# Kernel optimization log

Hardware: AMD Instinct MI355X
Metric: run time of the kernel (lower is better)

## Reference

```python
import jax, jax.numpy as jnp
import numpy as np

N_PE = 100000   # num 'pe' nodes
N_R = 100000    # num 'router' nodes
E = 600000      # edges per relation
D_IN = 64       # input feature dim per node type
H = 128         # hidden_channels
G = 64          # graphs in batch


def setup_inputs() -> dict:
    key = jax.random.key(0)
    ks = jax.random.split(key, 20)
    inp = {}
    inp["x_pe"] = jax.random.normal(ks[0], (N_PE, D_IN), jnp.float32)
    inp["x_r"] = jax.random.normal(ks[1], (N_R, D_IN), jnp.float32)
    # edge_index per relation: row0 = src node ids, row1 = dst node ids
    inp["ei_per"] = jax.random.randint(ks[2], (2, E), 0, N_PE, jnp.int32)   # pe -> router
    inp["ei_rpe"] = jax.random.randint(ks[3], (2, E), 0, N_R, jnp.int32)    # router -> pe
    inp["ei_rr"] = jax.random.randint(ks[4], (2, E), 0, N_R, jnp.int32)     # router -> router
    inp["batch_pe"] = jnp.sort(jax.random.randint(ks[5], (N_PE,), 0, G, jnp.int32))
    inp["batch_r"] = jnp.sort(jax.random.randint(ks[6], (N_R,), 0, G, jnp.int32))
    # GraphConv params, relation axis ordered [pe->router, router->pe, router->router]
    s1 = 1.0 / np.sqrt(D_IN)
    s2 = 1.0 / np.sqrt(H)
    inp["Wrel1"] = jax.random.normal(ks[7], (3, D_IN, H), jnp.float32) * s1
    inp["brel1"] = jnp.zeros((3, H), jnp.float32)
    inp["Wroot1"] = jax.random.normal(ks[8], (3, D_IN, H), jnp.float32) * s1
    inp["Wrel23"] = jax.random.normal(ks[9], (2, 3, H, H), jnp.float32) * s2
    inp["brel23"] = jnp.zeros((2, 3, H), jnp.float32)
    inp["Wroot23"] = jax.random.normal(ks[10], (2, 3, H, H), jnp.float32) * s2
    # per-node-type MLP heads, type axis ordered [pe, router]
    inp["mlp_W1"] = jax.random.normal(ks[11], (2, H, 5), jnp.float32) * s2
    inp["mlp_b1"] = jnp.zeros((2, 5), jnp.float32)
    inp["mlp_W2"] = jax.random.normal(ks[12], (2, 5, 1), jnp.float32) * (1.0 / np.sqrt(5.0))
    inp["mlp_b2"] = jnp.zeros((2, 1), jnp.float32)
    inp["out_W"] = jax.random.normal(ks[13], (2, 1), jnp.float32) * (1.0 / np.sqrt(2.0))
    inp["out_b"] = jnp.zeros((1,), jnp.float32)
    return inp


def _hetero_graphconv(x_pe, x_r, ei_per, ei_rpe, ei_rr, Wrel, brel, Wroot):
    # GraphConv: lin_rel(scatter_add(x_src)) + lin_root(x_dst); to_hetero sums per dst type.
    agg_r_from_pe = jax.ops.segment_sum(x_pe[ei_per[0]], ei_per[1], num_segments=N_R)
    agg_pe_from_r = jax.ops.segment_sum(x_r[ei_rpe[0]], ei_rpe[1], num_segments=N_PE)
    agg_r_from_r = jax.ops.segment_sum(x_r[ei_rr[0]], ei_rr[1], num_segments=N_R)
    o_pe = agg_pe_from_r @ Wrel[1] + brel[1] + x_pe @ Wroot[1]
    o_r = (agg_r_from_pe @ Wrel[0] + brel[0] + x_r @ Wroot[0]) \
        + (agg_r_from_r @ Wrel[2] + brel[2] + x_r @ Wroot[2])
    return o_pe, o_r


def reference(x_pe, x_r, ei_per, ei_rpe, ei_rr, batch_pe, batch_r,
              Wrel1, brel1, Wroot1, Wrel23, brel23, Wroot23,
              mlp_W1, mlp_b1, mlp_W2, mlp_b2, out_W, out_b):
    h_pe, h_r = _hetero_graphconv(x_pe, x_r, ei_per, ei_rpe, ei_rr, Wrel1, brel1, Wroot1)
    h_pe, h_r = jax.nn.relu(h_pe), jax.nn.relu(h_r)
    h_pe, h_r = _hetero_graphconv(h_pe, h_r, ei_per, ei_rpe, ei_rr, Wrel23[0], brel23[0], Wroot23[0])
    h_pe, h_r = jax.nn.relu(h_pe), jax.nn.relu(h_r)
    h_pe, h_r = _hetero_graphconv(h_pe, h_r, ei_per, ei_rpe, ei_rr, Wrel23[1], brel23[1], Wroot23[1])
    gm_pe = jax.ops.segment_max(h_pe, batch_pe, num_segments=G)  # [G, H]
    gm_r = jax.ops.segment_max(h_r, batch_r, num_segments=G)
    def mlp(x, W1, b1, W2, b2):
        return jax.nn.relu(x @ W1 + b1) @ W2 + b2
    o_pe = mlp(gm_pe, mlp_W1[0], mlp_b1[0], mlp_W2[0], mlp_b2[0])  # [G, 1]
    o_r = mlp(gm_r, mlp_W1[1], mlp_b1[1], mlp_W2[1], mlp_b2[1])
    cat = jnp.concatenate([o_pe, o_r], axis=1)  # [G, 2]
    return cat @ out_W + out_b  # [G, 1]
```

## Files before the change

kernel.cpp:

```cpp
#include <hip/hip_runtime.h>
#include <cstddef>
#include <cstdint>

#define DIN 64
#define HID 128
#define NBKMAX 256
#define EPB 2048

typedef _Float16 half4v __attribute__((ext_vector_type(4)));
typedef _Float16 half8v __attribute__((ext_vector_type(8)));
typedef float f32x16 __attribute__((ext_vector_type(16)));

__device__ __forceinline__ unsigned encf(float f) {
    unsigned b = __float_as_uint(f);
    return (b & 0x80000000u) ? ~b : (b | 0x80000000u);
}
__device__ __forceinline__ float decf(unsigned u) {
    unsigned b = (u & 0x80000000u) ? (u & 0x7FFFFFFFu) : ~u;
    return __uint_as_float(b);
}

__global__ void conv_x2_k(const float* s0, _Float16* d0, int n40,
                          const float* s1, _Float16* d1, int n41) {
    int r = blockIdx.y;
    const float* s = r == 0 ? s0 : s1;
    _Float16* d = r == 0 ? d0 : d1;
    int n4 = r == 0 ? n40 : n41;
    int i = blockIdx.x * 256 + threadIdx.x;
    if (i >= n4) return;
    float4 v = *reinterpret_cast<const float4*>(&s[i * 4]);
    half4v h;
    h.x = (_Float16)v.x; h.y = (_Float16)v.y; h.z = (_Float16)v.z; h.w = (_Float16)v.w;
    *reinterpret_cast<half4v*>(&d[i * 4]) = h;
}

struct CW { const float* src; const float* src2; _Float16* dst; int K; int total; };
__global__ void conv_w8_k(CW c0, CW c1, CW c2, CW c3, CW c4, CW c5, CW c6, CW c7) {
    CW J;
    switch (blockIdx.y) {
        case 0: J = c0; break; case 1: J = c1; break; case 2: J = c2; break;
        case 3: J = c3; break; case 4: J = c4; break; case 5: J = c5; break;
        case 6: J = c6; break; default: J = c7; break;
    }
    int i = blockIdx.x * 256 + threadIdx.x;
    if (i >= J.total) return;
    int m = i / (J.K * HID);
    int rem = i % (J.K * HID);
    int k = rem / HID;
    int col = rem % HID;
    float v = J.src[i];
    if (J.src2) v += J.src2[i];
    J.dst[(size_t)m * HID * J.K + (size_t)col * J.K + k] = (_Float16)v;
}

__global__ __launch_bounds__(256) void bhist_k(const int* e0, const int* e1, const int* e2, int E,
                                               int* c0, int* c1, int* c2) {
    int r = blockIdx.y;
    const int* ei = r == 0 ? e0 : (r == 1 ? e1 : e2);
    int* cnt = r == 0 ? c0 : (r == 1 ? c1 : c2);
    __shared__ int sc[NBKMAX];
    int t = threadIdx.x;
    sc[t] = 0;
    __syncthreads();
    int base = blockIdx.x * EPB;
    int n = min(EPB, E - base);
    for (int i = t; i < n; i += 256)
        atomicAdd(&sc[(unsigned)ei[E + base + i] >> 9], 1);
    __syncthreads();
    if (sc[t]) atomicAdd(&cnt[t], sc[t]);
}

__global__ __launch_bounds__(256) void bscan_k(int* c0, int* bb0, int* cu0, int* rp0, int n0,
                                               int* c1, int* bb1, int* cu1, int* rp1, int n1,
                                               int* c2, int* bb2, int* cu2, int* rp2, int n2,
                                               int E) {
    __shared__ int sh[256];
    int t = threadIdx.x;
    for (int r = 0; r < 3; ++r) {
        int* cnt = r == 0 ? c0 : (r == 1 ? c1 : c2);
        int* bb  = r == 0 ? bb0 : (r == 1 ? bb1 : bb2);
        int* cu  = r == 0 ? cu0 : (r == 1 ? cu1 : cu2);
        int* rp  = r == 0 ? rp0 : (r == 1 ? rp1 : rp2);
        int N    = r == 0 ? n0 : (r == 1 ? n1 : n2);
        int v = cnt[t];
        sh[t] = v;
        __syncthreads();
        for (int off = 1; off < 256; off <<= 1) {
            int val = (t >= off) ? sh[t - off] : 0;
            __syncthreads();
            sh[t] += val;
            __syncthreads();
        }
        int ex = sh[t] - v;
        bb[t] = ex;
        cu[t] = ex;
        if (t == 255) bb[256] = sh[255];
        if (t == 0) rp[N] = E;
        __syncthreads();
    }
}

__global__ __launch_bounds__(256) void bin_k(const int* e0, const int* e1, const int* e2, int E,
                                             int* cu0, int* cu1, int* cu2,
                                             unsigned* t0, unsigned* t1, unsigned* t2) {
    int r = blockIdx.y;
    const int* ei = r == 0 ? e0 : (r == 1 ? e1 : e2);
    int* gcur = r == 0 ? cu0 : (r == 1 ? cu1 : cu2);
    unsigned* temp = r == 0 ? t0 : (r == 1 ? t1 : t2);
    __shared__ unsigned pk[EPB];
    __shared__ unsigned short bkb[EPB];
    __shared__ int cnt[NBKMAX];
    __shared__ int scn[NBKMAX];
    __shared__ int rb[NBKMAX];
    int t = threadIdx.x;
    int base = blockIdx.x * EPB;
    int n = min(EPB, E - base);
    cnt[t] = 0;
    __syncthreads();
    for (int i = t; i < n; i += 256)
        atomicAdd(&cnt[(unsigned)ei[E + base + i] >> 9], 1);
    __syncthreads();
    {
        int v = cnt[t];
        scn[t] = v;
        __syncthreads();
        for (int off = 1; off < 256; off <<= 1) {
            int val = (t >= off) ? scn[t - off] : 0;
            __syncthreads();
            scn[t] += val;
            __syncthreads();
        }
        int ex = scn[t] - v;
        __syncthreads();
        scn[t] = ex;
    }
    {
        int c = cnt[t];
        rb[t] = c ? atomicAdd(&gcur[t], c) : 0;
        cnt[t] = 0;
    }
    __syncthreads();
    for (int i = t; i < n; i += 256) {
        int s = ei[base + i];
        int d = ei[E + base + i];
        int b = (unsigned)d >> 9;
        int slot = scn[b] + atomicAdd(&cnt[b], 1);
        pk[slot] = ((unsigned)s << 9) | (unsigned)(d & 511);
        bkb[slot] = (unsigned short)b;
    }
    __syncthreads();
    for (int i = t; i < n; i += 256) {
        int b = bkb[i];
        temp[rb[b] + (i - scn[b])] = pk[i];
    }
}

__global__ __launch_bounds__(256) void bcsr_k(const unsigned* t0, const unsigned* t1, const unsigned* t2,
                                              const int* bb0, const int* bb1, const int* bb2,
                                              int* rp0, int* rp1, int* rp2,
                                              int* a0, int* a1, int* a2,
                                              int n0, int n1, int n2) {
    int r = blockIdx.y;
    const unsigned* temp = r == 0 ? t0 : (r == 1 ? t1 : t2);
    const int* bb = r == 0 ? bb0 : (r == 1 ? bb1 : bb2);
    int* rp = r == 0 ? rp0 : (r == 1 ? rp1 : rp2);
    int* adj = r == 0 ? a0 : (r == 1 ? a1 : a2);
    int N = r == 0 ? n0 : (r == 1 ? n1 : n2);
    int b = blockIdx.x;
    int lo = bb[b], hi = bb[b + 1];
    __shared__ int cnt[512];
    __shared__ int sh[256];
    int t = threadIdx.x;
    cnt[t] = 0; cnt[t + 256] = 0;
    __syncthreads();
    for (int i = lo + t; i < hi; i += 256)
        atomicAdd(&cnt[temp[i] & 511], 1);
    __syncthreads();
    int c0 = cnt[2 * t], c1 = cnt[2 * t + 1];
    sh[t] = c0 + c1;
    __syncthreads();
    for (int off = 1; off < 256; off <<= 1) {
        int v = (t >= off) ? sh[t - off] : 0;
        __syncthreads();
        sh[t] += v;
        __syncthreads();
    }
    int pairExcl = sh[t] - (c0 + c1);
    __syncthreads();
    int e0x = lo + pairExcl;
    int e1x = e0x + c0;
    cnt[2 * t] = e0x;
    cnt[2 * t + 1] = e1x;
    int nodeBase = b * 512;
    if (nodeBase + 2 * t < N) rp[nodeBase + 2 * t] = e0x;
    if (nodeBase + 2 * t + 1 < N) rp[nodeBase + 2 * t + 1] = e1x;
    __syncthreads();
    for (int i = lo + t; i < hi; i += 256) {
        unsigned p = temp[i];
        int pos = atomicAdd(&cnt[p & 511], 1);
        adj[pos] = p >> 9;
    }
}

struct AJob { const _Float16* X; const int* rp; const int* adj; _Float16* AGG; int N; int gb; };
template <int D>
__global__ __launch_bounds__(256) void gather3_k(AJob a0, AJob a1, AJob a2) {
    int b = blockIdx.x;
    AJob J;
    if (b < a0.gb) { J = a0; }
    else if (b < a0.gb + a1.gb) { J = a1; b -= a0.gb; }
    else { J = a2; b -= a0.gb + a1.gb; }
    constexpr int TPN = D / 8;
    constexpr int NPB = 256 / TPN;
    int node = b * NPB + threadIdx.x / TPN;
    int glane = threadIdx.x % TPN;
    if (node >= J.N) return;
    int a = J.rp[node], e1 = J.rp[node + 1];
    float acc[8] = {0.f, 0.f, 0.f, 0.f, 0.f, 0.f, 0.f, 0.f};
    for (int base = a; base < e1; base += TPN) {
        int idx = base + glane;
        int myAdj = (idx < e1) ? J.adj[idx] : 0;
        int cnt = min(TPN, e1 - base);
        int j = 0;
        for (; j + 4 <= cnt; j += 4) {
            int s0 = __shfl(myAdj, j, TPN);
            int s1 = __shfl(myAdj, j + 1, TPN);
            int s2 = __shfl(myAdj, j + 2, TPN);
            int s3 = __shfl(myAdj, j + 3, TPN);
            half8v v0 = *reinterpret_cast<const half8v*>(&J.X[(size_t)s0 * D + glane * 8]);
            half8v v1 = *reinterpret_cast<const half8v*>(&J.X[(size_t)s1 * D + glane * 8]);
            half8v v2 = *reinterpret_cast<const half8v*>(&J.X[(size_t)s2 * D + glane * 8]);
            half8v v3 = *reinterpret_cast<const half8v*>(&J.X[(size_t)s3 * D + glane * 8]);
#pragma unroll
            for (int i = 0; i < 8; ++i)
                acc[i] += (float)v0[i] + (float)v1[i] + (float)v2[i] + (float)v3[i];
        }
        for (; j < cnt; ++j) {
            int s0 = __shfl(myAdj, j, TPN);
            half8v v0 = *reinterpret_cast<const half8v*>(&J.X[(size_t)s0 * D + glane * 8]);
#pragma unroll
            for (int i = 0; i < 8; ++i) acc[i] += (float)v0[i];
        }
    }
    half8v o;
#pragma unroll
    for (int i = 0; i < 8; ++i) o[i] = (_Float16)acc[i];
    *reinterpret_cast<half8v*>(&J.AGG[(size_t)node * D + glane * 8]) = o;
}

struct GJob {
    const _Float16* A0; const _Float16* A1; const _Float16* A2;
    const _Float16* W0; const _Float16* W1; const _Float16* W2;
    const float* b0; const float* b1;
    _Float16* O;
    int N; int total; int gb;
};

template <bool RELU>
__global__ __launch_bounds__(256) void gemm2_k(GJob j0, GJob j1, int K, int lg) {
    const bool second = ((int)blockIdx.x >= j0.gb);
    const GJob J = second ? j1 : j0;
    const int bx = blockIdx.x - (second ? j0.gb : 0);
    __shared__ _Float16 Alds[128 * 64];
    __shared__ _Float16 Wlds[128 * 64];
    const int tid = threadIdx.x;
    const int lane = tid & 63;
    const int w = tid >> 6;
    const int wr = w & 1, wc = w >> 1;
    const int rowBase = bx * 128;

    f32x16 acc[2][2];
#pragma unroll
    for (int r = 0; r < 2; ++r)
#pragma unroll
        for (int c = 0; c < 2; ++c)
#pragma unroll
            for (int q = 0; q < 16; ++q) acc[r][c][q] = 0.0f;

    const _Float16* Ap[3] = {J.A0, J.A1, J.A2};

    const int row = tid & 127;
    const int kh = (tid >> 7) * 32;
    const int gr = rowBase + row;
    const bool rowOK = (gr < J.N);
    int offS[4];
#pragma unroll
    for (int j = 0; j < 4; ++j) {
        int t = (kh >> 4) + (j >> 1);
        int k8 = j & 1;
        offS[j] = (((row >> 5) * 4 + t) * 64 + (row & 31) + 32 * k8) * 8;
    }

    const int total = J.total;
    const int cmask = (1 << lg) - 1;

    auto ldA = [&](int c, half8v h[4]) {
        int s = c >> lg;
        int k0 = (c & cmask) * 64;
        half8v z = {};
        h[0] = z; h[1] = z; h[2] = z; h[3] = z;
        if (rowOK) {
            const _Float16* p = Ap[s] + (size_t)gr * K + k0 + kh;
#pragma unroll
            for (int j = 0; j < 4; ++j) h[j] = *reinterpret_cast<const half8v*>(p + j * 8);
        }
    };
    auto ldW = [&](int c, half8v h[4]) {
        int s = c >> lg;
        int k0 = (c & cmask) * 64;
        const _Float16* __restrict__ Wt = (s == 0) ? J.W0 : (s == 1 ? J.W1 : J.W2);
        const _Float16* p = Wt + (size_t)row * K + k0 + kh;
#pragma unroll
        for (int j = 0; j < 4; ++j) h[j] = *reinterpret_cast<const half8v*>(p + j * 8);
    };

    half8v ra[4], rw[4];
    ldA(0, ra); ldW(0, rw);
#pragma unroll
    for (int j = 0; j < 4; ++j) {
        *reinterpret_cast<half8v*>(&Alds[offS[j]]) = ra[j];
        *reinterpret_cast<half8v*>(&Wlds[offS[j]]) = rw[j];
    }
    __syncthreads();

    for (int c = 0; c < total; ++c) {
        const bool more = (c + 1 < total);
        if (more) { ldA(c + 1, ra); ldW(c + 1, rw); }
#pragma unroll
        for (int t = 0; t < 4; ++t) {
            half8v av[2], wv[2];
#pragma unroll
            for (int r = 0; r < 2; ++r)
                av[r] = *reinterpret_cast<const half8v*>(&Alds[(((wr * 2 + r) * 4 + t) * 64 + lane) * 8]);
#pragma unroll
            for (int cc = 0; cc < 2; ++cc)
                wv[cc] = *reinterpret_cast<const half8v*>(&Wlds[(((wc * 2 + cc) * 4 + t) * 64 + lane) * 8]);
#pragma unroll
            for (int r = 0; r < 2; ++r)
#pragma unroll
                for (int cc = 0; cc < 2; ++cc)
                    acc[r][cc] = __builtin_amdgcn_mfma_f32_32x32x16_f16(wv[cc], av[r], acc[r][cc], 0, 0, 0);
        }
        __syncthreads();
        if (more) {
#pragma unroll
            for (int j = 0; j < 4; ++j) {
                *reinterpret_cast<half8v*>(&Alds[offS[j]]) = ra[j];
                *reinterpret_cast<half8v*>(&Wlds[offS[j]]) = rw[j];
            }
            __syncthreads();
        }
    }

    const int half_ = lane >> 5;
#pragma unroll
    for (int r = 0; r < 2; ++r) {
        int node = rowBase + (wr * 2 + r) * 32 + (lane & 31);
        bool ok = (node < J.N);
        _Float16* orow = J.O + (size_t)node * HID;
#pragma unroll
        for (int cc = 0; cc < 2; ++cc) {
            int fbase = wc * 64 + cc * 32;
#pragma unroll
            for (int g = 0; g < 4; ++g) {
                int fmine = fbase + g * 8 + 4 * half_;
                float4 bv = *reinterpret_cast<const float4*>(&J.b0[fmine]);
                if (J.b1) {
                    float4 b2v = *reinterpret_cast<const float4*>(&J.b1[fmine]);
                    bv.x += b2v.x; bv.y += b2v.y; bv.z += b2v.z; bv.w += b2v.w;
                }
                union { half4v h; int i[2]; } m, p;
#pragma unroll
                for (int i = 0; i < 4; ++i) {
                    float v = acc[r][cc][g * 4 + i] + ((const float*)&bv)[i];
                    if (RELU) v = fmaxf(v, 0.f);
                    m.h[i] = (_Float16)v;
                }
                p.i[0] = __shfl_xor(m.i[0], 32);
                p.i[1] = __shfl_xor(m.i[1], 32);
                half4v lo = half_ ? p.h : m.h;
                half4v hi = half_ ? m.h : p.h;
                half8v outv;
#pragma unroll
                for (int i = 0; i < 4; ++i) { outv[i] = lo[i]; outv[4 + i] = hi[i]; }
                if (ok && ((g & 1) == half_))
                    *reinterpret_cast<half8v*>(&orow[fbase + g * 8]) = outv;
            }
        }
    }
}

__global__ void seg_bounds2_k(const int* b0, int n0, int* s0,
                              const int* b1, int n1, int* s1, int G) {
    int r = blockIdx.x;
    const int* batch = r == 0 ? b0 : b1;
    int n = r == 0 ? n0 : n1;
    int* starts = r == 0 ? s0 : s1;
    int g = threadIdx.x;
    if (g > G) return;
    int lo = 0, hi = n;
    while (lo < hi) {
        int mid = (lo + hi) >> 1;
        if (batch[mid] < g) lo = mid + 1; else hi = mid;
    }
    starts[g] = lo;
}

__global__ __launch_bounds__(128) void seg_max2_k(const _Float16* H0, const int* st0, unsigned* g0,
                                                  const _Float16* H1, const int* st1, unsigned* g1) {
    int z = blockIdx.z;
    const _Float16* Hf = z == 0 ? H0 : H1;
    const int* starts = z == 0 ? st0 : st1;
    unsigned* gmU = z == 0 ? g0 : g1;
    int g = blockIdx.x;
    int sub = blockIdx.y;
    int SUB = gridDim.y;
    int f = threadIdx.x;
    int s0 = starts[g], s1 = starts[g + 1];
    int len = s1 - s0;
    if (len <= 0) return;
    int chunk = (len + SUB - 1) / SUB;
    int a = s0 + sub * chunk;
    int b = min(a + chunk, s1);
    if (a >= b) return;
    float m = -__builtin_huge_valf();
    for (int n = a; n < b; ++n) m = fmaxf(m, (float)Hf[(size_t)n * HID + f]);
    atomicMax(&gmU[g * HID + f], encf(m));
}

__global__ void head_k(const unsigned* __restrict__ gmU_pe, const unsigned* __restrict__ gmU_r,
                       const float* __restrict__ W1, const float* __restrict__ b1,
                       const float* __restrict__ W2, const float* __restrict__ b2,
                       const float* __restrict__ oW, const float* __restrict__ ob,
                       float* __restrict__ out, int G) {
    int g = threadIdx.x;
    if (g >= G) return;
    float vals[2];
#pragma unroll
    for (int t = 0; t < 2; ++t) {
        const unsigned* gm = t ? gmU_r : gmU_pe;
        float z[5];
#pragma unroll
        for (int j = 0; j < 5; ++j) z[j] = b1[t * 5 + j];
        for (int f = 0; f < HID; ++f) {
            float x = decf(gm[g * HID + f]);
#pragma unroll
            for (int j = 0; j < 5; ++j) z[j] = fmaf(x, W1[t * HID * 5 + f * 5 + j], z[j]);
        }
        float o = b2[t];
#pragma unroll
        for (int j = 0; j < 5; ++j) o = fmaf(fmaxf(z[j], 0.f), W2[t * 5 + j], o);
        vals[t] = o;
    }
    out[g] = vals[0] * oW[0] + vals[1] * oW[1] + ob[0];
}

extern "C" void kernel_launch(void* const* d_in, const int* in_sizes, int n_in,
                              void* d_out, int out_size, void* d_ws, size_t ws_size,
                              hipStream_t stream) {
    const float* x_pe    = (const float*)d_in[0];
    const float* x_r     = (const float*)d_in[1];
    const int* ei_per    = (const int*)d_in[2];
    const int* ei_rpe    = (const int*)d_in[3];
    const int* ei_rr     = (const int*)d_in[4];
    const int* batch_pe  = (const int*)d_in[5];
    const int* batch_r   = (const int*)d_in[6];
    const float* Wrel1   = (const float*)d_in[7];
    const float* brel1   = (const float*)d_in[8];
    const float* Wroot1  = (const float*)d_in[9];
    const float* Wrel23  = (const float*)d_in[10];
    const float* brel23  = (const float*)d_in[11];
    const float* Wroot23 = (const float*)d_in[12];
    const float* mlp_W1  = (const float*)d_in[13];
    const float* mlp_b1  = (const float*)d_in[14];
    const float* mlp_W2  = (const float*)d_in[15];
    const float* mlp_b2  = (const float*)d_in[16];
    const float* out_W   = (const float*)d_in[17];
    const float* out_b   = (const float*)d_in[18];
    float* out = (float*)d_out;

    const int N_PE = in_sizes[0] / DIN;
    const int N_R  = in_sizes[1] / DIN;
    const int E    = in_sizes[2] / 2;
    const int G    = out_size;
    const int NMAX = (N_PE > N_R) ? N_PE : N_R;
    const size_t SZM = (size_t)NMAX * HID;

    _Float16* H1 = (_Float16*)d_ws;
    _Float16* H2 = H1 + SZM;
    _Float16* H3 = H2 + SZM;
    _Float16* H4 = H3 + SZM;
    _Float16* H5 = H4 + SZM;
    _Float16* xh_pe = H5 + SZM;
    _Float16* xh_r  = xh_pe + (size_t)N_PE * DIN;
    _Float16* wt_rel1    = xh_r + (size_t)N_R * DIN;
    _Float16* wt_root1pe = wt_rel1 + 3 * DIN * HID;
    _Float16* wt_wsum1   = wt_root1pe + DIN * HID;
    _Float16* wt_rel23   = wt_wsum1 + DIN * HID;
    _Float16* wt_root_l2 = wt_rel23 + 6 * HID * HID;
    _Float16* wt_root_l3 = wt_root_l2 + HID * HID;
    _Float16* wt_wsum2   = wt_root_l3 + HID * HID;
    _Float16* wt_wsum3   = wt_wsum2 + HID * HID;
    unsigned* gmU_pe = (unsigned*)(wt_wsum3 + HID * HID);
    unsigned* gmU_r  = gmU_pe + G * HID;
    int* starts_pe = (int*)(gmU_r + G * HID);
    int* starts_r  = starts_pe + (G + 1);
    int* bktCnt = starts_r + (G + 1);
    int* bb     = bktCnt + 3 * NBKMAX;
    int* gcur   = bb + 3 * (NBKMAX + 1);
    int* csr    = gcur + 3 * NBKMAX;
    const size_t relstride = (size_t)(NMAX + 1) + 2 * (size_t)E + 16;

    int* rp[3]; int* adjp[3]; unsigned* tmp[3];
    const int Nds[3] = {N_R, N_PE, N_R};
    for (int r = 0; r < 3; ++r) {
        int* rowptr = csr + (size_t)r * relstride;
        rp[r] = rowptr;
        adjp[r] = rowptr + (Nds[r] + 1);
        tmp[r] = (unsigned*)(adjp[r] + E);
    }

    const int gpe = (N_PE + 127) / 128, grr = (N_R + 127) / 128;

    {
        int n40 = N_PE * DIN / 4, n41 = N_R * DIN / 4;
        int nmax = n40 > n41 ? n40 : n41;
        dim3 g((nmax + 255) / 256, 2);
        conv_x2_k<<<g, 256, 0, stream>>>(x_pe, xh_pe, n40, x_r, xh_r, n41);
    }
    {
        CW c0{Wrel1, nullptr, wt_rel1, DIN, 3 * DIN * HID};
        CW c1{Wroot1 + 1 * DIN * HID, nullptr, wt_root1pe, DIN, DIN * HID};
        CW c2{Wroot1, Wroot1 + 2 * DIN * HID, wt_wsum1, DIN, DIN * HID};
        CW c3{Wrel23, nullptr, wt_rel23, HID, 6 * HID * HID};
        CW c4{Wroot23 + 1 * HID * HID, nullptr, wt_root_l2, HID, HID * HID};
        CW c5{Wroot23 + 4 * HID * HID, nullptr, wt_root_l3, HID, HID * HID};
        CW c6{Wroot23, Wroot23 + 2 * HID * HID, wt_wsum2, HID, HID * HID};
        CW c7{Wroot23 + 3 * HID * HID, Wroot23 + 5 * HID * HID, wt_wsum3, HID, HID * HID};
        dim3 g((6 * HID * HID + 255) / 256, 8);
        conv_w8_k<<<g, 256, 0, stream>>>(c0, c1, c2, c3, c4, c5, c6, c7);
    }
    {
        hipMemsetAsync(bktCnt, 0, 3 * NBKMAX * sizeof(int), stream);
        int eb = (E + EPB - 1) / EPB;
        dim3 gh(eb, 3);
        bhist_k<<<gh, 256, 0, stream>>>(ei_per, ei_rpe, ei_rr, E,
                                        bktCnt, bktCnt + NBKMAX, bktCnt + 2 * NBKMAX);
        bscan_k<<<1, 256, 0, stream>>>(
            bktCnt, bb, gcur, rp[0], Nds[0],
            bktCnt + NBKMAX, bb + (NBKMAX + 1), gcur + NBKMAX, rp[1], Nds[1],
            bktCnt + 2 * NBKMAX, bb + 2 * (NBKMAX + 1), gcur + 2 * NBKMAX, rp[2], Nds[2], E);
        bin_k<<<gh, 256, 0, stream>>>(ei_per, ei_rpe, ei_rr, E,
                                      gcur, gcur + NBKMAX, gcur + 2 * NBKMAX,
                                      tmp[0], tmp[1], tmp[2]);
        dim3 gc(NBKMAX, 3);
        bcsr_k<<<gc, 256, 0, stream>>>(tmp[0], tmp[1], tmp[2],
                                       bb, bb + (NBKMAX + 1), bb + 2 * (NBKMAX + 1),
                                       rp[0], rp[1], rp[2],
                                       adjp[0], adjp[1], adjp[2],
                                       Nds[0], Nds[1], Nds[2]);
    }

    {
        AJob a0{xh_r, rp[1], adjp[1], H1, N_PE, (N_PE + 31) / 32};
        AJob a1{xh_pe, rp[0], adjp[0], H2, N_R, (N_R + 31) / 32};
        AJob a2{xh_r, rp[2], adjp[2], H3, N_R, (N_R + 31) / 32};
        gather3_k<DIN><<<a0.gb + a1.gb + a2.gb, 256, 0, stream>>>(a0, a1, a2);
        GJob jp{H1, xh_pe, nullptr,
                wt_rel1 + 1 * DIN * HID, wt_root1pe, nullptr,
                brel1 + HID, nullptr, H4, N_PE, 2, gpe};
        GJob jr{H2, H3, xh_r,
                wt_rel1, wt_rel1 + 2 * DIN * HID, wt_wsum1,
                brel1, brel1 + 2 * HID, H5, N_R, 3, grr};
        gemm2_k<true><<<gpe + grr, 256, 0, stream>>>(jp, jr, DIN, 0);
    }
    {
        AJob a0{H5, rp[1], adjp[1], H1, N_PE, (N_PE + 15) / 16};
        AJob a1{H4, rp[0], adjp[0], H2, N_R, (N_R + 15) / 16};
        AJob a2{H5, rp[2], adjp[2], H3, N_R, (N_R + 15) / 16};
        gather3_k<HID><<<a0.gb + a1.gb + a2.gb, 256, 0, stream>>>(a0, a1, a2);
        GJob jp{H1, H4, nullptr,
                wt_rel23 + 1 * HID * HID, wt_root_l2, nullptr,
                brel23 + HID, nullptr, H1, N_PE, 2 * 2, gpe};
        GJob jr{H2, H3, H5,
                wt_rel23, wt_rel23 + 2 * HID * HID, wt_wsum2,
                brel23, brel23 + 2 * HID, H2, N_R, 3 * 2, grr};
        gemm2_k<true><<<gpe + grr, 256, 0, stream>>>(jp, jr, HID, 1);
    }
    {
        AJob a0{H2, rp[1], adjp[1], H3, N_PE, (N_PE + 15) / 16};
        AJob a1{H1, rp[0], adjp[0], H4, N_R, (N_R + 15) / 16};
        AJob a2{H2, rp[2], adjp[2], H5, N_R, (N_R + 15) / 16};
        gather3_k<HID><<<a0.gb + a1.gb + a2.gb, 256, 0, stream>>>(a0, a1, a2);
        GJob jp{H3, H1, nullptr,
                wt_rel23 + 4 * HID * HID, wt_root_l3, nullptr,
                brel23 + 4 * HID, nullptr, H3, N_PE, 2 * 2, gpe};
        GJob jr{H4, H5, H2,
                wt_rel23 + 3 * HID * HID, wt_rel23 + 5 * HID * HID, wt_wsum3,
                brel23 + 3 * HID, brel23 + 5 * HID, H4, N_R, 3 * 2, grr};
        gemm2_k<false><<<gpe + grr, 256, 0, stream>>>(jp, jr, HID, 1);
    }

    seg_bounds2_k<<<2, 128, 0, stream>>>(batch_pe, N_PE, starts_pe, batch_r, N_R, starts_r, G);
    hipMemsetAsync(gmU_pe, 0, 2 * (size_t)G * HID * sizeof(unsigned), stream);
    dim3 gs(G, 16, 2);
    seg_max2_k<<<gs, 128, 0, stream>>>(H3, starts_pe, gmU_pe, H4, starts_r, gmU_r);
    head_k<<<1, 64, 0, stream>>>(gmU_pe, gmU_r, mlp_W1, mlp_b1, mlp_W2, mlp_b2, out_W, out_b, out, G);
}
```

Baseline: 619.0 us.

## Fuse prep kernels and split GEMM tile across eight waves

Merges weight conversion, edge bucket histogram and segment-bounds search into a single prep kernel. Two memsets become one by moving the bucket counters next to the max buffers. The GEMM goes from 256 to 512 threads per 128x128 tile, so each wave owns a 64x32 sub-tile with two accumulators instead of four, which cuts register pressure and adds waves to hide latency. The cost is less reuse of each LDS fragment per wave and more barrier participants, with the same LDS footprint per block.

```diff
diff --git a/kernel.cpp b/kernel.cpp
--- a/kernel.cpp
+++ b/kernel.cpp
@@ -35,39 +35,59 @@
 }
 
 struct CW { const float* src; const float* src2; _Float16* dst; int K; int total; };
-__global__ void conv_w8_k(CW c0, CW c1, CW c2, CW c3, CW c4, CW c5, CW c6, CW c7) {
-    CW J;
-    switch (blockIdx.y) {
-        case 0: J = c0; break; case 1: J = c1; break; case 2: J = c2; break;
-        case 3: J = c3; break; case 4: J = c4; break; case 5: J = c5; break;
-        case 6: J = c6; break; default: J = c7; break;
-    }
-    int i = blockIdx.x * 256 + threadIdx.x;
-    if (i >= J.total) return;
-    int m = i / (J.K * HID);
-    int rem = i % (J.K * HID);
-    int k = rem / HID;
-    int col = rem % HID;
-    float v = J.src[i];
-    if (J.src2) v += J.src2[i];
-    J.dst[(size_t)m * HID * J.K + (size_t)col * J.K + k] = (_Float16)v;
-}
-
-__global__ __launch_bounds__(256) void bhist_k(const int* e0, const int* e1, const int* e2, int E,
-                                               int* c0, int* c1, int* c2) {
-    int r = blockIdx.y;
-    const int* ei = r == 0 ? e0 : (r == 1 ? e1 : e2);
-    int* cnt = r == 0 ? c0 : (r == 1 ? c1 : c2);
-    __shared__ int sc[NBKMAX];
-    int t = threadIdx.x;
-    sc[t] = 0;
-    __syncthreads();
-    int base = blockIdx.x * EPB;
-    int n = min(EPB, E - base);
-    for (int i = t; i < n; i += 256)
-        atomicAdd(&sc[(unsigned)ei[E + base + i] >> 9], 1);
-    __syncthreads();
-    if (sc[t]) atomicAdd(&cnt[t], sc[t]);
+__global__ __launch_bounds__(256) void prep_k(
+    CW c0, CW c1, CW c2, CW c3, CW c4, CW c5, CW c6, CW c7,
+    const int* e0, const int* e1, const int* e2, int E,
+    int* hc0, int* hc1, int* hc2,
+    const int* bpe, int npe, int* spe,
+    const int* brr, int nrr, int* srr, int G) {
+    int y = blockIdx.y;
+    if (y < 8) {
+        CW J;
+        switch (y) {
+            case 0: J = c0; break; case 1: J = c1; break; case 2: J = c2; break;
+            case 3: J = c3; break; case 4: J = c4; break; case 5: J = c5; break;
+            case 6: J = c6; break; default: J = c7; break;
+        }
+        int i = blockIdx.x * 256 + threadIdx.x;
+        if (i >= J.total) return;
+        int m = i / (J.K * HID);
+        int rem = i % (J.K * HID);
+        int k = rem / HID;
+        int col = rem % HID;
+        float v = J.src[i];
+        if (J.src2) v += J.src2[i];
+        J.dst[(size_t)m * HID * J.K + (size_t)col * J.K + k] = (_Float16)v;
+    } else if (y < 11) {
+        int r = y - 8;
+        const int* ei = r == 0 ? e0 : (r == 1 ? e1 : e2);
+        int* cnt = r == 0 ? hc0 : (r == 1 ? hc1 : hc2);
+        __shared__ int sc[NBKMAX];
+        int t = threadIdx.x;
+        sc[t] = 0;
+        __syncthreads();
+        int base = blockIdx.x * EPB;
+        if (base >= E) return;
+        int n = min(EPB, E - base);
+        for (int i = t; i < n; i += 256)
+            atomicAdd(&sc[(unsigned)ei[E + base + i] >> 9], 1);
+        __syncthreads();
+        if (sc[t]) atomicAdd(&cnt[t], sc[t]);
+    } else {
+        int r = blockIdx.x;
+        if (r >= 2) return;
+        const int* batch = r == 0 ? bpe : brr;
+        int n = r == 0 ? npe : nrr;
+        int* starts = r == 0 ? spe : srr;
+        int g = threadIdx.x;
+        if (g > G) return;
+        int lo = 0, hi = n;
+        while (lo < hi) {
+            int mid = (lo + hi) >> 1;
+            if (batch[mid] < g) lo = mid + 1; else hi = mid;
+        }
+        starts[g] = lo;
+    }
 }
 
 __global__ __launch_bounds__(256) void bscan_k(int* c0, int* bb0, int* cu0, int* rp0, int n0,
@@ -257,7 +277,7 @@
 };
 
 template <bool RELU>
-__global__ __launch_bounds__(256) void gemm2_k(GJob j0, GJob j1, int K, int lg) {
+__global__ __launch_bounds__(512) void gemm2_k(GJob j0, GJob j1, int K, int lg) {
     const bool second = ((int)blockIdx.x >= j0.gb);
     const GJob J = second ? j1 : j0;
     const int bx = blockIdx.x - (second ? j0.gb : 0);
@@ -266,58 +286,54 @@
     const int tid = threadIdx.x;
     const int lane = tid & 63;
     const int w = tid >> 6;
-    const int wr = w & 1, wc = w >> 1;
+    const int wr = w & 1;
+    const int wc = w >> 1;
     const int rowBase = bx * 128;
 
-    f32x16 acc[2][2];
+    f32x16 acc[2];
 #pragma unroll
     for (int r = 0; r < 2; ++r)
 #pragma unroll
-        for (int c = 0; c < 2; ++c)
-#pragma unroll
-            for (int q = 0; q < 16; ++q) acc[r][c][q] = 0.0f;
+        for (int q = 0; q < 16; ++q) acc[r][q] = 0.0f;
 
     const _Float16* Ap[3] = {J.A0, J.A1, J.A2};
 
     const int row = tid & 127;
-    const int kh = (tid >> 7) * 32;
+    const int kq = (tid >> 7) * 16;
     const int gr = rowBase + row;
     const bool rowOK = (gr < J.N);
-    int offS[4];
-#pragma unroll
-    for (int j = 0; j < 4; ++j) {
-        int t = (kh >> 4) + (j >> 1);
-        int k8 = j & 1;
-        offS[j] = (((row >> 5) * 4 + t) * 64 + (row & 31) + 32 * k8) * 8;
-    }
+    int offS[2];
+#pragma unroll
+    for (int j = 0; j < 2; ++j)
+        offS[j] = (((row >> 5) * 4 + (kq >> 4)) * 64 + (row & 31) + 32 * j) * 8;
 
     const int total = J.total;
     const int cmask = (1 << lg) - 1;
 
-    auto ldA = [&](int c, half8v h[4]) {
+    auto ldA = [&](int c, half8v h[2]) {
         int s = c >> lg;
         int k0 = (c & cmask) * 64;
         half8v z = {};
-        h[0] = z; h[1] = z; h[2] = z; h[3] = z;
+        h[0] = z; h[1] = z;
         if (rowOK) {
-            const _Float16* p = Ap[s] + (size_t)gr * K + k0 + kh;
-#pragma unroll
-            for (int j = 0; j < 4; ++j) h[j] = *reinterpret_cast<const half8v*>(p + j * 8);
+            const _Float16* p = Ap[s] + (size_t)gr * K + k0 + kq;
+            h[0] = *reinterpret_cast<const half8v*>(p);
+            h[1] = *reinterpret_cast<const half8v*>(p + 8);
         }
     };
-    auto ldW = [&](int c, half8v h[4]) {
+    auto ldW = [&](int c, half8v h[2]) {
         int s = c >> lg;
         int k0 = (c & cmask) * 64;
         const _Float16* __restrict__ Wt = (s == 0) ? J.W0 : (s == 1 ? J.W1 : J.W2);
-        const _Float16* p = Wt + (size_t)row * K + k0 + kh;
-#pragma unroll
-        for (int j = 0; j < 4; ++j) h[j] = *reinterpret_cast<const half8v*>(p + j * 8);
+        const _Float16* p = Wt + (size_t)row * K + k0 + kq;
+        h[0] = *reinterpret_cast<const half8v*>(p);
+        h[1] = *reinterpret_cast<const half8v*>(p + 8);
     };
 
-    half8v ra[4], rw[4];
+    half8v ra[2], rw[2];
     ldA(0, ra); ldW(0, rw);
 #pragma unroll
-    for (int j = 0; j < 4; ++j) {
+    for (int j = 0; j < 2; ++j) {
         *reinterpret_cast<half8v*>(&Alds[offS[j]]) = ra[j];
         *reinterpret_cast<half8v*>(&Wlds[offS[j]]) = rw[j];
     }
@@ -328,23 +344,18 @@
         if (more) { ldA(c + 1, ra); ldW(c + 1, rw); }
 #pragma unroll
         for (int t = 0; t < 4; ++t) {
-            half8v av[2], wv[2];
-#pragma unroll
-            for (int r = 0; r < 2; ++r)
-                av[r] = *reinterpret_cast<const half8v*>(&Alds[(((wr * 2 + r) * 4 + t) * 64 + lane) * 8]);
-#pragma unroll
-            for (int cc = 0; cc < 2; ++cc)
-                wv[cc] = *reinterpret_cast<const half8v*>(&Wlds[(((wc * 2 + cc) * 4 + t) * 64 + lane) * 8]);
-#pragma unroll
-            for (int r = 0; r < 2; ++r)
-#pragma unroll
-                for (int cc = 0; cc < 2; ++cc)
-                    acc[r][cc] = __builtin_amdgcn_mfma_f32_32x32x16_f16(wv[cc], av[r], acc[r][cc], 0, 0, 0);
+            half8v wv = *reinterpret_cast<const half8v*>(&Wlds[((wc * 4 + t) * 64 + lane) * 8]);
+#pragma unroll
+            for (int r = 0; r < 2; ++r) {
+                half8v av = *reinterpret_cast<const half8v*>(
+                    &Alds[(((wr * 2 + r) * 4 + t) * 64 + lane) * 8]);
+                acc[r] = __builtin_amdgcn_mfma_f32_32x32x16_f16(wv, av, acc[r], 0, 0, 0);
+            }
         }
         __syncthreads();
         if (more) {
 #pragma unroll
-            for (int j = 0; j < 4; ++j) {
+            for (int j = 0; j < 2; ++j) {
                 *reinterpret_cast<half8v*>(&Alds[offS[j]]) = ra[j];
                 *reinterpret_cast<half8v*>(&Wlds[offS[j]]) = rw[j];
             }
@@ -353,57 +364,38 @@
     }
 
     const int half_ = lane >> 5;
+    const int fbase = wc * 32;
 #pragma unroll
     for (int r = 0; r < 2; ++r) {
         int node = rowBase + (wr * 2 + r) * 32 + (lane & 31);
         bool ok = (node < J.N);
         _Float16* orow = J.O + (size_t)node * HID;
 #pragma unroll
-        for (int cc = 0; cc < 2; ++cc) {
-            int fbase = wc * 64 + cc * 32;
-#pragma unroll
-            for (int g = 0; g < 4; ++g) {
-                int fmine = fbase + g * 8 + 4 * half_;
-                float4 bv = *reinterpret_cast<const float4*>(&J.b0[fmine]);
-                if (J.b1) {
-                    float4 b2v = *reinterpret_cast<const float4*>(&J.b1[fmine]);
-                    bv.x += b2v.x; bv.y += b2v.y; bv.z += b2v.z; bv.w += b2v.w;
-                }
-                union { half4v h; int i[2]; } m, p;
-#pragma unroll
-                for (int i = 0; i < 4; ++i) {
-                    float v = acc[r][cc][g * 4 + i] + ((const float*)&bv)[i];
-                    if (RELU) v = fmaxf(v, 0.f);
-                    m.h[i] = (_Float16)v;
-                }
-                p.i[0] = __shfl_xor(m.i[0], 32);
-                p.i[1] = __shfl_xor(m.i[1], 32);
-                half4v lo = half_ ? p.h : m.h;
-                half4v hi = half_ ? m.h : p.h;
-                half8v outv;
-#pragma unroll
-                for (int i = 0; i < 4; ++i) { outv[i] = lo[i]; outv[4 + i] = hi[i]; }
-                if (ok && ((g & 1) == half_))
-                    *reinterpret_cast<half8v*>(&orow[fbase + g * 8]) = outv;
+        for (int g = 0; g < 4; ++g) {
+            int fmine = fbase + g * 8 + 4 * half_;
+            float4 bv = *reinterpret_cast<const float4*>(&J.b0[fmine]);
+            if (J.b1) {
+                float4 b2v = *reinterpret_cast<const float4*>(&J.b1[fmine]);
+                bv.x += b2v.x; bv.y += b2v.y; bv.z += b2v.z; bv.w += b2v.w;
             }
-        }
-    }
-}
-
-__global__ void seg_bounds2_k(const int* b0, int n0, int* s0,
-                              const int* b1, int n1, int* s1, int G) {
-    int r = blockIdx.x;
-    const int* batch = r == 0 ? b0 : b1;
-    int n = r == 0 ? n0 : n1;
-    int* starts = r == 0 ? s0 : s1;
-    int g = threadIdx.x;
-    if (g > G) return;
-    int lo = 0, hi = n;
-    while (lo < hi) {
-        int mid = (lo + hi) >> 1;
-        if (batch[mid] < g) lo = mid + 1; else hi = mid;
-    }
-    starts[g] = lo;
+            union { half4v h; int i[2]; } m, p;
+#pragma unroll
+            for (int i = 0; i < 4; ++i) {
+                float v = acc[r][g * 4 + i] + ((const float*)&bv)[i];
+                if (RELU) v = fmaxf(v, 0.f);
+                m.h[i] = (_Float16)v;
+            }
+            p.i[0] = __shfl_xor(m.i[0], 32);
+            p.i[1] = __shfl_xor(m.i[1], 32);
+            half4v lo = half_ ? p.h : m.h;
+            half4v hi = half_ ? m.h : p.h;
+            half8v outv;
+#pragma unroll
+            for (int i = 0; i < 4; ++i) { outv[i] = lo[i]; outv[4 + i] = hi[i]; }
+            if (ok && ((g & 1) == half_))
+                *reinterpret_cast<half8v*>(&orow[fbase + g * 8]) = outv;
+        }
+    }
 }
 
 __global__ __launch_bounds__(128) void seg_max2_k(const _Float16* H0, const int* st0, unsigned* g0,
@@ -503,10 +495,10 @@
     _Float16* wt_wsum3   = wt_wsum2 + HID * HID;
     unsigned* gmU_pe = (unsigned*)(wt_wsum3 + HID * HID);
     unsigned* gmU_r  = gmU_pe + G * HID;
-    int* starts_pe = (int*)(gmU_r + G * HID);
+    int* bktCnt = (int*)(gmU_r + G * HID);
+    int* starts_pe = bktCnt + 3 * NBKMAX;
     int* starts_r  = starts_pe + (G + 1);
-    int* bktCnt = starts_r + (G + 1);
-    int* bb     = bktCnt + 3 * NBKMAX;
+    int* bb     = starts_r + (G + 1);
     int* gcur   = bb + 3 * (NBKMAX + 1);
     int* csr    = gcur + 3 * NBKMAX;
     const size_t relstride = (size_t)(NMAX + 1) + 2 * (size_t)E + 16;
@@ -521,7 +513,9 @@
     }
 
     const int gpe = (N_PE + 127) / 128, grr = (N_R + 127) / 128;
-
+    const int eb = (E + EPB - 1) / EPB;
+
+    hipMemsetAsync(gmU_pe, 0, (2 * (size_t)G * HID + 3 * NBKMAX) * sizeof(int), stream);
     {
         int n40 = N_PE * DIN / 4, n41 = N_R * DIN / 4;
         int nmax = n40 > n41 ? n40 : n41;
@@ -537,19 +531,21 @@
         CW c5{Wroot23 + 4 * HID * HID, nullptr, wt_root_l3, HID, HID * HID};
         CW c6{Wroot23, Wroot23 + 2 * HID * HID, wt_wsum2, HID, HID * HID};
         CW c7{Wroot23 + 3 * HID * HID, Wroot23 + 5 * HID * HID, wt_wsum3, HID, HID * HID};
-        dim3 g((6 * HID * HID + 255) / 256, 8);
-        conv_w8_k<<<g, 256, 0, stream>>>(c0, c1, c2, c3, c4, c5, c6, c7);
-    }
-    {
-        hipMemsetAsync(bktCnt, 0, 3 * NBKMAX * sizeof(int), stream);
-        int eb = (E + EPB - 1) / EPB;
-        dim3 gh(eb, 3);
-        bhist_k<<<gh, 256, 0, stream>>>(ei_per, ei_rpe, ei_rr, E,
-                                        bktCnt, bktCnt + NBKMAX, bktCnt + 2 * NBKMAX);
+        int gx = (6 * HID * HID + 255) / 256;
+        if (eb > gx) gx = eb;
+        dim3 g(gx, 12);
+        prep_k<<<g, 256, 0, stream>>>(c0, c1, c2, c3, c4, c5, c6, c7,
+                                      ei_per, ei_rpe, ei_rr, E,
+                                      bktCnt, bktCnt + NBKMAX, bktCnt + 2 * NBKMAX,
+                                      batch_pe, N_PE, starts_pe,
+                                      batch_r, N_R, starts_r, G);
+    }
+    {
         bscan_k<<<1, 256, 0, stream>>>(
             bktCnt, bb, gcur, rp[0], Nds[0],
             bktCnt + NBKMAX, bb + (NBKMAX + 1), gcur + NBKMAX, rp[1], Nds[1],
             bktCnt + 2 * NBKMAX, bb + 2 * (NBKMAX + 1), gcur + 2 * NBKMAX, rp[2], Nds[2], E);
+        dim3 gh(eb, 3);
         bin_k<<<gh, 256, 0, stream>>>(ei_per, ei_rpe, ei_rr, E,
                                       gcur, gcur + NBKMAX, gcur + 2 * NBKMAX,
                                       tmp[0], tmp[1], tmp[2]);
@@ -572,7 +568,7 @@
         GJob jr{H2, H3, xh_r,
                 wt_rel1, wt_rel1 + 2 * DIN * HID, wt_wsum1,
                 brel1, brel1 + 2 * HID, H5, N_R, 3, grr};
-        gemm2_k<true><<<gpe + grr, 256, 0, stream>>>(jp, jr, DIN, 0);
+        gemm2_k<true><<<gpe + grr, 512, 0, stream>>>(jp, jr, DIN, 0);
     }
     {
         AJob a0{H5, rp[1], adjp[1], H1, N_PE, (N_PE + 15) / 16};
@@ -585,7 +581,7 @@
         GJob jr{H2, H3, H5,
                 wt_rel23, wt_rel23 + 2 * HID * HID, wt_wsum2,
                 brel23, brel23 + 2 * HID, H2, N_R, 3 * 2, grr};
-        gemm2_k<true><<<gpe + grr, 256, 0, stream>>>(jp, jr, HID, 1);
+        gemm2_k<true><<<gpe + grr, 512, 0, stream>>>(jp, jr, HID, 1);
     }
     {
         AJob a0{H2, rp[1], adjp[1], H3, N_PE, (N_PE + 15) / 16};
@@ -598,11 +594,9 @@
         GJob jr{H4, H5, H2,
                 wt_rel23 + 3 * HID * HID, wt_rel23 + 5 * HID * HID, wt_wsum3,
                 brel23 + 3 * HID, brel23 + 5 * HID, H4, N_R, 3 * 2, grr};
-        gemm2_k<false><<<gpe + grr, 256, 0, stream>>>(jp, jr, HID, 1);
-    }
-
-    seg_bounds2_k<<<2, 128, 0, stream>>>(batch_pe, N_PE, starts_pe, batch_r, N_R, starts_r, G);
-    hipMemsetAsync(gmU_pe, 0, 2 * (size_t)G * HID * sizeof(unsigned), stream);
+        gemm2_k<false><<<gpe + grr, 512, 0, stream>>>(jp, jr, HID, 1);
+    }
+
     dim3 gs(G, 16, 2);
     seg_max2_k<<<gs, 128, 0, stream>>>(H3, starts_pe, gmU_pe, H4, starts_r, gmU_r);
     head_k<<<1, 64, 0, stream>>>(gmU_pe, gmU_r, mlp_W1, mlp_b1, mlp_W2, mlp_b2, out_W, out_b, out, G);
```

After: 611.3 us. Within noise of the previous version (-1.2%).
